# Performance work log

Measured on AMD Instinct MI355X. Metric: run time of the kernel, lower is better.

Reference implementation:

```python
import jax, jax.numpy as jnp
import numpy as np

B, N, D_IN, D_HID, D_OUT = 8, 512, 4608, 4608, 1152
DROP = 0.1
INV_SQRT2 = 0.7071067811865476
INV_SQRT_2PI = 0.3989422804014327


def _clean(s):
    # nan -> 1e-5, inf -> 1.0 (matches torch.where chain)
    return jnp.where(jnp.isnan(s), jnp.asarray(1e-5, s.dtype),
                     jnp.where(jnp.isinf(s), jnp.asarray(1.0, s.dtype), s))


def kl_regularizer(w_mu, w_sigma):
    d = w_mu.shape[0]
    ws = jax.nn.softplus(w_sigma)  # log(1+exp(w_sigma))
    return 0.5 * jnp.mean(d * ws + jnp.sum(w_mu * w_mu, axis=0) - d - d * jnp.log(ws))


def vdp_linear(mu_in, Sigma_in, w_mu, w_sigma):
    mu_out = jnp.matmul(mu_in, w_mu)                                 # [B,N,U]
    kl = kl_regularizer(w_mu, w_sigma)
    W_Sigma = jax.nn.softplus(w_sigma)                               # [U]
    Sigma_1 = jnp.matmul(Sigma_in, w_mu * w_mu)                      # w^T Sigma_in w (diag)
    Sigma_2 = jnp.sum(mu_in * mu_in, axis=-1, keepdims=True) * W_Sigma
    Sigma_3 = jnp.sum(Sigma_in, axis=-1, keepdims=True) * W_Sigma
    return mu_out, _clean(Sigma_1 + Sigma_2 + Sigma_3), kl


def vdp_gelu(mu_in, Sigma_in):
    # exact (erf) gelu and its analytic derivative: Phi(x) + x*phi(x)
    cdf = 0.5 * (1.0 + jax.lax.erf(mu_in * INV_SQRT2))
    pdf = jnp.exp(-0.5 * mu_in * mu_in) * INV_SQRT_2PI
    grad = cdf + mu_in * pdf
    return mu_in * cdf, grad * grad * Sigma_in


def vdp_dropout(mu_in, Sigma_in, mask):
    keep = 1.0 - DROP
    m = mask.astype(mu_in.dtype)
    mu_out = mu_in * m / keep                       # torch F.dropout scaling
    Sigma_out = Sigma_in * m / mu_in.shape[-1]      # kept Sigma values (unscaled), / units
    return mu_out, _clean(Sigma_out)


def setup_inputs() -> dict:
    key = jax.random.key(0)
    k = jax.random.split(key, 8)
    mu_in = jax.random.normal(k[0], (B, N, D_IN), dtype=jnp.float32)
    sigma_in = jax.random.uniform(k[1], (B, N, D_IN), dtype=jnp.float32)
    mask1 = jax.random.bernoulli(k[2], 1.0 - DROP, (B, N, D_HID))
    mask2 = jax.random.bernoulli(k[3], 1.0 - DROP, (B, N, D_OUT))
    w_mu1 = 0.05 * jax.random.normal(k[4], (D_IN, D_HID), dtype=jnp.float32)
    w_sigma1 = jnp.full((D_HID,), -4.6, dtype=jnp.float32)
    w_mu2 = 0.05 * jax.random.normal(k[5], (D_HID, D_OUT), dtype=jnp.float32)
    w_sigma2 = jnp.full((D_OUT,), -4.6, dtype=jnp.float32)
    return {"mu_in": mu_in, "sigma_in": sigma_in, "mask1": mask1, "mask2": mask2,
            "w_mu1": w_mu1, "w_sigma1": w_sigma1, "w_mu2": w_mu2, "w_sigma2": w_sigma2}


def reference(mu_in, sigma_in, mask1, mask2, w_mu1, w_sigma1, w_mu2, w_sigma2):
    mu, sig, kl1 = vdp_linear(mu_in, sigma_in, w_mu1, w_sigma1)
    mu, sig = vdp_gelu(mu, sig)
    mu, sig = vdp_dropout(mu, sig, mask1)
    mu, sig, kl2 = vdp_linear(mu, sig, w_mu2, w_sigma2)
    mu, sig = vdp_dropout(mu, sig, mask2)
    return mu, _clean(sig), kl1 + kl2
```

## Files before the change

kernel.cpp:

```cpp
#include <hip/hip_runtime.h>
#include <cstdint>
#include <cstddef>

static constexpr int Mrows = 4096;
static constexpr int K1 = 4608;
static constexpr int N1 = 4608;
static constexpr int N2 = 1152;
static constexpr int SPLITK = 2;
static constexpr int NPART1 = (K1 / 32) * (N1 / 32);
static constexpr int NPART2 = (K1 / 32) * (N2 / 32);

static constexpr float SC_SIGIN = 256.f;
static constexpr float SC_WSQ   = 4096.f;
static constexpr float SC_SIG3  = 16384.f;
static constexpr float DSC_L1   = 1.f / (SC_SIGIN * SC_WSQ);
static constexpr float DSC_L2   = 1.f / (SC_SIG3 * SC_WSQ);

typedef float  f32x4  __attribute__((ext_vector_type(4)));
typedef __bf16 bf16x8 __attribute__((ext_vector_type(8)));

__device__ __forceinline__ unsigned short f2bf(float f) {
  unsigned int u = __float_as_uint(f);
  u += 0x7fffu + ((u >> 16) & 1u);
  return (unsigned short)(u >> 16);
}
__device__ __forceinline__ float bf2f(unsigned short h) {
  return __uint_as_float(((unsigned int)h) << 16);
}
__device__ __forceinline__ float cleanf(float s) {
  if (__builtin_isnan(s)) return 1e-5f;
  if (__builtin_isinf(s)) return 1.0f;
  return s;
}
__device__ __forceinline__ unsigned int pk_fp8x4(float a, float b, float c, float d) {
  int p = __builtin_amdgcn_cvt_pk_fp8_f32(a, b, 0, false);
  p = __builtin_amdgcn_cvt_pk_fp8_f32(c, d, p, true);
  return (unsigned int)p;
}

__global__ __launch_bounds__(256) void prep_in(
    const float* __restrict__ mu, const float* __restrict__ sg,
    unsigned short* __restrict__ A1, unsigned char* __restrict__ As,
    float* __restrict__ rmu2, float* __restrict__ rsg)
{
  const int row = blockIdx.x;
  const int tid = threadIdx.x;
  const float4* mup = (const float4*)(mu + (size_t)row * K1);
  const float4* sgp = (const float4*)(sg + (size_t)row * K1);
  ushort4* a1p = (ushort4*)(A1 + (size_t)row * K1);
  unsigned int* asp = (unsigned int*)(As + (size_t)row * K1);
  float smu = 0.f, ssg = 0.f;
  for (int j = tid; j < K1 / 4; j += 256) {
    float4 m4 = mup[j];
    float4 s4 = sgp[j];
    smu += m4.x*m4.x + m4.y*m4.y + m4.z*m4.z + m4.w*m4.w;
    ssg += s4.x + s4.y + s4.z + s4.w;
    a1p[j] = make_ushort4(f2bf(m4.x), f2bf(m4.y), f2bf(m4.z), f2bf(m4.w));
    asp[j] = pk_fp8x4(s4.x * SC_SIGIN, s4.y * SC_SIGIN, s4.z * SC_SIGIN, s4.w * SC_SIGIN);
  }
  __shared__ float red[2][4];
  for (int off = 32; off; off >>= 1) {
    smu += __shfl_down(smu, off);
    ssg += __shfl_down(ssg, off);
  }
  const int lane = tid & 63, wv = tid >> 6;
  if (!lane) { red[0][wv] = smu; red[1][wv] = ssg; }
  __syncthreads();
  if (tid == 0) {
    rmu2[row] = red[0][0] + red[0][1] + red[0][2] + red[0][3];
    rsg[row]  = red[1][0] + red[1][1] + red[1][2] + red[1][3];
  }
}

__global__ __launch_bounds__(256) void prep_w(
    const float* __restrict__ w, unsigned short* __restrict__ Bt,
    unsigned char* __restrict__ Bsq, float* __restrict__ partials,
    int K, int N)
{
  __shared__ float t[32][33];
  const int kt = blockIdx.x * 32;
  const int nt = blockIdx.y * 32;
  const int tx = threadIdx.x & 31;
  const int ty = threadIdx.x >> 5;
  float loc = 0.f;
#pragma unroll
  for (int i = 0; i < 32; i += 8) {
    float v = w[(size_t)(kt + ty + i) * N + (nt + tx)];
    t[ty + i][tx] = v;
    loc += v * v;
  }
  __syncthreads();
#pragma unroll
  for (int i = 0; i < 32; i += 8) {
    float v = t[tx][ty + i];
    size_t o = (size_t)(nt + ty + i) * K + (kt + tx);
    Bt[o]  = f2bf(v);
    Bsq[o] = (unsigned char)(__builtin_amdgcn_cvt_pk_fp8_f32(v * v * SC_WSQ, 0.f, 0, false) & 0xff);
  }
  __shared__ float red[4];
  for (int off = 32; off; off >>= 1) loc += __shfl_down(loc, off);
  const int lane = threadIdx.x & 63, wv = threadIdx.x >> 6;
  if (!lane) red[wv] = loc;
  __syncthreads();
  if (threadIdx.x == 0)
    partials[blockIdx.y * gridDim.x + blockIdx.x] = red[0] + red[1] + red[2] + red[3];
}

__global__ __launch_bounds__(256) void kl_prep(
    const float* __restrict__ wsig1, const float* __restrict__ wsig2,
    const float* __restrict__ part1, const float* __restrict__ part2,
    float* __restrict__ ws1, float* __restrict__ ws2, float* __restrict__ outkl)
{
  const int tid = threadIdx.x;
  float s1 = 0.f, l1 = 0.f, s2 = 0.f, l2 = 0.f, q1 = 0.f, q2 = 0.f;
  for (int j = tid; j < N1; j += 256) {
    float x = wsig1[j];
    float sp = (x > 20.f) ? x : log1pf(expf(x));
    ws1[j] = sp; s1 += sp; l1 += logf(sp);
  }
  for (int j = tid; j < N2; j += 256) {
    float x = wsig2[j];
    float sp = (x > 20.f) ? x : log1pf(expf(x));
    ws2[j] = sp; s2 += sp; l2 += logf(sp);
  }
  for (int j = tid; j < NPART1; j += 256) q1 += part1[j];
  for (int j = tid; j < NPART2; j += 256) q2 += part2[j];
  __shared__ float red[6][4];
  for (int off = 32; off; off >>= 1) {
    s1 += __shfl_down(s1, off); l1 += __shfl_down(l1, off);
    s2 += __shfl_down(s2, off); l2 += __shfl_down(l2, off);
    q1 += __shfl_down(q1, off); q2 += __shfl_down(q2, off);
  }
  const int lane = tid & 63, wv = tid >> 6;
  if (!lane) {
    red[0][wv] = s1; red[1][wv] = l1; red[2][wv] = s2;
    red[3][wv] = l2; red[4][wv] = q1; red[5][wv] = q2;
  }
  __syncthreads();
  if (tid == 0) {
    float S1v = red[0][0] + red[0][1] + red[0][2] + red[0][3];
    float L1v = red[1][0] + red[1][1] + red[1][2] + red[1][3];
    float S2v = red[2][0] + red[2][1] + red[2][2] + red[2][3];
    float L2v = red[3][0] + red[3][1] + red[3][2] + red[3][3];
    float Q1v = red[4][0] + red[4][1] + red[4][2] + red[4][3];
    float Q2v = red[5][0] + red[5][1] + red[5][2] + red[5][3];
    const float d = 4608.f;
    float kl1 = 0.5f * (d * (S1v / (float)N1) + Q1v / (float)N1 - d - d * (L1v / (float)N1));
    float kl2 = 0.5f * (d * (S2v / (float)N2) + Q2v / (float)N2 - d - d * (L2v / (float)N2));
    outkl[0] = kl1 + kl2;
  }
}

#define GLD16(gp, lp) __builtin_amdgcn_global_load_lds( \
    (__attribute__((address_space(1))) void*)(unsigned short*)(gp), \
    (__attribute__((address_space(3))) void*)(lp), 16, 0, 0)

__device__ __forceinline__ void storeC(float v, float* p) { *p = v; }
__device__ __forceinline__ void storeC(float v, unsigned short* p) { *p = f2bf(v); }

template <typename CT>
__global__ __launch_bounds__(256) void gemm_bt2(
    const unsigned short* __restrict__ Aa, const unsigned char* __restrict__ As8,
    const unsigned short* __restrict__ Ba, const unsigned char* __restrict__ Bq8,
    CT* __restrict__ Ca, CT* __restrict__ Cs,
    int M, int N, int Kstride, int Klen, float sdescale)
{
  __shared__ __align__(16) char smem[32768];
  const int tid = threadIdx.x;
  const int lane = tid & 63;
  const int wave = tid >> 6;

  const int which = blockIdx.z & 1;
  const int slice = blockIdx.z >> 1;

  const int m0 = blockIdx.y * 128;
  const int n0 = blockIdx.x * 128;
  const int wm = (wave & 1) * 64;
  const int wn = (wave >> 1) * 64;

  const int fm = lane & 15;
  const int kq = lane >> 4;

  f32x4 acc[4][4];
#pragma unroll
  for (int i = 0; i < 4; i++)
#pragma unroll
    for (int j = 0; j < 4; j++) acc[i][j] = (f32x4){0.f, 0.f, 0.f, 0.f};

  if (which == 0) {
    const unsigned short* A  = Aa + (size_t)slice * Klen;
    const unsigned short* Bt = Ba + (size_t)slice * Klen;
    unsigned short* lA = (unsigned short*)smem;
    unsigned short* lB = (unsigned short*)(smem + 16384);

    const int c0 = tid, c1 = tid + 256;
    const int r0s = c0 >> 2, k0s = (c0 & 3) ^ ((r0s >> 1) & 3);
    const int r1s = c1 >> 2, k1s = (c1 & 3) ^ ((r1s >> 1) & 3);
    const unsigned short* gA0 = A + (size_t)(m0 + r0s) * Kstride + k0s * 8;
    const unsigned short* gA1 = A + (size_t)(m0 + r1s) * Kstride + k1s * 8;
    const unsigned short* gB0 = Bt + (size_t)(n0 + r0s) * Kstride + k0s * 8;
    const unsigned short* gB1 = Bt + (size_t)(n0 + r1s) * Kstride + k1s * 8;

    int aoff[4], boff[4];
#pragma unroll
    for (int i = 0; i < 4; i++) {
      int ra = wm + i * 16 + fm;
      aoff[i] = ra * 32 + ((kq ^ ((ra >> 1) & 3)) * 8);
      int rb = wn + i * 16 + fm;
      boff[i] = rb * 32 + ((kq ^ ((rb >> 1) & 3)) * 8);
    }

    GLD16(gA0, &lA[c0 * 8]); GLD16(gA1, &lA[c1 * 8]);
    GLD16(gB0, &lB[c0 * 8]); GLD16(gB1, &lB[c1 * 8]);
    gA0 += 32; gA1 += 32; gB0 += 32; gB1 += 32;

    const int ksteps = Klen >> 5;
    int cur = 0;
    for (int kt = 0; kt < ksteps; kt++) {
      __syncthreads();
      if (kt + 1 < ksteps) {
        const int nb = cur ^ 1;
        GLD16(gA0, &lA[nb * 4096 + c0 * 8]); GLD16(gA1, &lA[nb * 4096 + c1 * 8]);
        GLD16(gB0, &lB[nb * 4096 + c0 * 8]); GLD16(gB1, &lB[nb * 4096 + c1 * 8]);
        gA0 += 32; gA1 += 32; gB0 += 32; gB1 += 32;
      }
      bf16x8 af[4], bfr[4];
#pragma unroll
      for (int i = 0; i < 4; i++) af[i] = *(const bf16x8*)&lA[cur * 4096 + aoff[i]];
#pragma unroll
      for (int i = 0; i < 4; i++) bfr[i] = *(const bf16x8*)&lB[cur * 4096 + boff[i]];
#pragma unroll
      for (int i = 0; i < 4; i++)
#pragma unroll
        for (int j = 0; j < 4; j++)
          acc[i][j] = __builtin_amdgcn_mfma_f32_16x16x32_bf16(af[i], bfr[j], acc[i][j], 0, 0, 0);
      cur ^= 1;
    }

    CT* C = Ca + (size_t)slice * M * N;
    const int rr = (lane >> 4) * 4;
    const int cc = lane & 15;
#pragma unroll
    for (int i = 0; i < 4; i++) {
      const int grow = m0 + wm + i * 16 + rr;
#pragma unroll
      for (int j = 0; j < 4; j++) {
        const int gcol = n0 + wn + j * 16 + cc;
        CT* cp = C + (size_t)grow * N + gcol;
#pragma unroll
        for (int r = 0; r < 4; r++) storeC(acc[i][j][r], cp + (size_t)r * N);
      }
    }
  } else {
    const unsigned char* A  = As8 + (size_t)slice * Klen;
    const unsigned char* Bt = Bq8 + (size_t)slice * Klen;
    char* lA = smem;
    char* lB = smem + 16384;

    const int s1 = tid, s2 = tid + 256;
    const int r1 = s1 & 127, h1 = s1 >> 7;
    const int r2 = s2 & 127, h2 = s2 >> 7;
    const unsigned char* gA0 = A + (size_t)(m0 + r1) * Kstride + h1 * 16;
    const unsigned char* gA1 = A + (size_t)(m0 + r2) * Kstride + h2 * 16;
    const unsigned char* gB0 = Bt + (size_t)(n0 + r1) * Kstride + h1 * 16;
    const unsigned char* gB1 = Bt + (size_t)(n0 + r2) * Kstride + h2 * 16;

    int aoff8[2][4], boff8[2][4];
#pragma unroll
    for (int hh = 0; hh < 2; hh++)
#pragma unroll
      for (int i = 0; i < 4; i++) {
        const int c = hh * 4 + kq;
        aoff8[hh][i] = (c >> 1) * 2048 + (wm + i * 16 + fm) * 16 + (c & 1) * 8;
        boff8[hh][i] = (c >> 1) * 2048 + (wn + i * 16 + fm) * 16 + (c & 1) * 8;
      }

    GLD16(gA0, lA + s1 * 16); GLD16(gA1, lA + s2 * 16);
    GLD16(gB0, lB + s1 * 16); GLD16(gB1, lB + s2 * 16);
    gA0 += 64; gA1 += 64; gB0 += 64; gB1 += 64;

    const int ksteps = Klen >> 6;
    int cur = 0;
    for (int kt = 0; kt < ksteps; kt++) {
      __syncthreads();
      if (kt + 1 < ksteps) {
        const int nb = cur ^ 1;
        GLD16(gA0, lA + nb * 8192 + s1 * 16); GLD16(gA1, lA + nb * 8192 + s2 * 16);
        GLD16(gB0, lB + nb * 8192 + s1 * 16); GLD16(gB1, lB + nb * 8192 + s2 * 16);
        gA0 += 64; gA1 += 64; gB0 += 64; gB1 += 64;
      }
#pragma unroll
      for (int hh = 0; hh < 2; hh++) {
        long av[4], bv[4];
#pragma unroll
        for (int i = 0; i < 4; i++) av[i] = *(const long*)(lA + cur * 8192 + aoff8[hh][i]);
#pragma unroll
        for (int i = 0; i < 4; i++) bv[i] = *(const long*)(lB + cur * 8192 + boff8[hh][i]);
#pragma unroll
        for (int i = 0; i < 4; i++)
#pragma unroll
          for (int j = 0; j < 4; j++)
            acc[i][j] = __builtin_amdgcn_mfma_f32_16x16x32_fp8_fp8(av[i], bv[j], acc[i][j], 0, 0, 0);
      }
      cur ^= 1;
    }

    CT* C = Cs + (size_t)slice * M * N;
    const int rr = (lane >> 4) * 4;
    const int cc = lane & 15;
#pragma unroll
    for (int i = 0; i < 4; i++) {
      const int grow = m0 + wm + i * 16 + rr;
#pragma unroll
      for (int j = 0; j < 4; j++) {
        const int gcol = n0 + wn + j * 16 + cc;
        CT* cp = C + (size_t)grow * N + gcol;
#pragma unroll
        for (int r = 0; r < 4; r++) storeC(acc[i][j][r] * sdescale, cp + (size_t)r * N);
      }
    }
  }
}

__global__ __launch_bounds__(256) void mid_kernel(
    const unsigned short* __restrict__ mu1, const unsigned short* __restrict__ S1,
    const int* __restrict__ mask1, const float* __restrict__ ws1,
    const float* __restrict__ rmu2, const float* __restrict__ rsg,
    unsigned short* __restrict__ A2, unsigned char* __restrict__ As2,
    float* __restrict__ r2mu, float* __restrict__ r2sg)
{
  const int row = blockIdx.x;
  const int tid = threadIdx.x;
  const float rterm = rmu2[row] + rsg[row];
  const ushort4* mup = (const ushort4*)(mu1 + (size_t)row * N1);
  const ushort4* s1p = (const ushort4*)(S1 + (size_t)row * N1);
  const int4* mkp = (const int4*)(mask1 + (size_t)row * N1);
  const float4* wsp = (const float4*)ws1;
  ushort4* a2p = (ushort4*)(A2 + (size_t)row * N1);
  unsigned int* as2p = (unsigned int*)(As2 + (size_t)row * N1);
  float smu = 0.f, ssg = 0.f;
  for (int j = tid; j < N1 / 4; j += 256) {
    ushort4 m4 = mup[j]; ushort4 s4 = s1p[j]; int4 k4 = mkp[j]; float4 w4 = wsp[j];
    float xv[4] = {bf2f(m4.x), bf2f(m4.y), bf2f(m4.z), bf2f(m4.w)};
    float Sv[4] = {bf2f(s4.x), bf2f(s4.y), bf2f(s4.z), bf2f(s4.w)};
    float wv[4] = {w4.x, w4.y, w4.z, w4.w};
    int   kv[4] = {k4.x, k4.y, k4.z, k4.w};
    unsigned short oa[4];
    float os[4];
#pragma unroll
    for (int t = 0; t < 4; t++) {
      float sig1 = cleanf(Sv[t] + rterm * wv[t]);
      float x = xv[t];
      float cdf = 0.5f * (1.f + erff(x * 0.70710678118654752f));
      float pdf = expf(-0.5f * x * x) * 0.3989422804014327f;
      float g = cdf + x * pdf;
      float mu2v = x * cdf;
      float sig2 = g * g * sig1;
      float mm = (float)kv[t];
      float mu3 = mu2v * mm * (1.f / 0.9f);
      float sig3 = cleanf(sig2 * mm * (1.f / 4608.f));
      smu += mu3 * mu3;
      ssg += sig3;
      oa[t] = f2bf(mu3);
      os[t] = sig3 * SC_SIG3;
    }
    a2p[j] = make_ushort4(oa[0], oa[1], oa[2], oa[3]);
    as2p[j] = pk_fp8x4(os[0], os[1], os[2], os[3]);
  }
  __shared__ float red[2][4];
  for (int off = 32; off; off >>= 1) {
    smu += __shfl_down(smu, off);
    ssg += __shfl_down(ssg, off);
  }
  const int lane = tid & 63, wv2 = tid >> 6;
  if (!lane) { red[0][wv2] = smu; red[1][wv2] = ssg; }
  __syncthreads();
  if (tid == 0) {
    r2mu[row] = red[0][0] + red[0][1] + red[0][2] + red[0][3];
    r2sg[row] = red[1][0] + red[1][1] + red[1][2] + red[1][3];
  }
}

__global__ __launch_bounds__(256) void final_kernel(
    const float* __restrict__ pmu, const float* __restrict__ psig,
    const int* __restrict__ mask2, const float* __restrict__ ws2,
    const float* __restrict__ r2mu, const float* __restrict__ r2sg,
    float* __restrict__ out_mu, float* __restrict__ out_sig)
{
  const int row = blockIdx.x;
  const int tid = threadIdx.x;
  const float rterm = r2mu[row] + r2sg[row];
  const size_t sstride = (size_t)Mrows * N2;
  const float4* mup0 = (const float4*)(pmu + (size_t)row * N2);
  const float4* sbp0 = (const float4*)(psig + (size_t)row * N2);
  const int4* mkp = (const int4*)(mask2 + (size_t)row * N2);
  const float4* wsp = (const float4*)ws2;
  float4* omp = (float4*)(out_mu + (size_t)row * N2);
  float4* osp = (float4*)(out_sig + (size_t)row * N2);
  const size_t s4 = sstride / 4;
  for (int j = tid; j < N2 / 4; j += 256) {
    float4 m4 = mup0[j];
    float4 sb = sbp0[j];
#pragma unroll
    for (int s = 1; s < SPLITK; s++) {
      float4 a = mup0[j + s * s4];
      float4 b = sbp0[j + s * s4];
      m4.x += a.x; m4.y += a.y; m4.z += a.z; m4.w += a.w;
      sb.x += b.x; sb.y += b.y; sb.z += b.z; sb.w += b.w;
    }
    int4 k4 = mkp[j]; float4 w4 = wsp[j];
    float mo[4], so[4];
    float mv[4] = {m4.x, m4.y, m4.z, m4.w};
    float sv[4] = {sb.x, sb.y, sb.z, sb.w};
    float wv[4] = {w4.x, w4.y, w4.z, w4.w};
    int   kv[4] = {k4.x, k4.y, k4.z, k4.w};
#pragma unroll
    for (int t = 0; t < 4; t++) {
      float sig4 = cleanf(sv[t] + rterm * wv[t]);
      float mm = (float)kv[t];
      float mu5 = mv[t] * mm * (1.f / 0.9f);
      float sig5 = cleanf(sig4 * mm * (1.f / 1152.f));
      mo[t] = mu5;
      so[t] = cleanf(sig5);
    }
    omp[j] = make_float4(mo[0], mo[1], mo[2], mo[3]);
    osp[j] = make_float4(so[0], so[1], so[2], so[3]);
  }
}

extern "C" void kernel_launch(void* const* d_in, const int* in_sizes, int n_in,
                              void* d_out, int out_size, void* d_ws, size_t ws_size,
                              hipStream_t stream)
{
  const float* mu_in = (const float*)d_in[0];
  const float* sg_in = (const float*)d_in[1];
  const int* mask1 = (const int*)d_in[2];
  const int* mask2 = (const int*)d_in[3];
  const float* w_mu1 = (const float*)d_in[4];
  const float* wsig1 = (const float*)d_in[5];
  const float* w_mu2 = (const float*)d_in[6];
  const float* wsig2 = (const float*)d_in[7];
  float* out = (float*)d_out;

  char* ws = (char*)d_ws;
  const size_t oA1  = 0;
  const size_t oAs  = oA1  + (size_t)37748736;
  const size_t oB1t = oAs  + (size_t)37748736;
  const size_t oB1q = oB1t + (size_t)42467328;
  const size_t oB2t = oB1q + (size_t)42467328;
  const size_t oB2q = oB2t + (size_t)10616832;
  const size_t oMu1 = oB2q + (size_t)10616832;
  const size_t oS1  = oMu1 + (size_t)37748736;
  const size_t oVec = oS1  + (size_t)37748736;

  unsigned short* A1    = (unsigned short*)(ws + oA1);
  unsigned char*  As8   = (unsigned char*)(ws + oAs);
  unsigned short* B1t   = (unsigned short*)(ws + oB1t);
  unsigned char*  B1q8  = (unsigned char*)(ws + oB1q);
  unsigned short* B2t   = (unsigned short*)(ws + oB2t);
  unsigned char*  B2q8  = (unsigned char*)(ws + oB2q);
  unsigned short* mu1b  = (unsigned short*)(ws + oMu1);
  unsigned short* S1b16 = (unsigned short*)(ws + oS1);
  float* pmu  = (float*)(ws + oB1t);
  float* psig = (float*)(ws + oMu1);

  float* rmu2 = (float*)(ws + oVec);
  float* rsg  = rmu2 + Mrows;
  float* r2mu = rsg + Mrows;
  float* r2sg = r2mu + Mrows;
  float* ws1v = r2sg + Mrows;
  float* ws2v = ws1v + N1;
  float* part1 = ws2v + N2;
  float* part2 = part1 + NPART1;

  prep_in<<<Mrows, 256, 0, stream>>>(mu_in, sg_in, A1, As8, rmu2, rsg);
  prep_w<<<dim3(K1 / 32, N1 / 32), 256, 0, stream>>>(w_mu1, B1t, B1q8, part1, K1, N1);
  prep_w<<<dim3(K1 / 32, N2 / 32), 256, 0, stream>>>(w_mu2, B2t, B2q8, part2, K1, N2);
  kl_prep<<<1, 256, 0, stream>>>(wsig1, wsig2, part1, part2, ws1v, ws2v,
                                 out + (size_t)2 * Mrows * N2);

  gemm_bt2<unsigned short><<<dim3(N1 / 128, Mrows / 128, 2), 256, 0, stream>>>(
      A1, As8, B1t, B1q8, mu1b, S1b16, Mrows, N1, K1, K1, DSC_L1);

  mid_kernel<<<Mrows, 256, 0, stream>>>(mu1b, S1b16, mask1, ws1v, rmu2, rsg,
                                        A1, As8, r2mu, r2sg);

  gemm_bt2<float><<<dim3(N2 / 128, Mrows / 128, 2 * SPLITK), 256, 0, stream>>>(
      A1, As8, B2t, B2q8, pmu, psig, Mrows, N2, K1, K1 / SPLITK, DSC_L2);

  final_kernel<<<Mrows, 256, 0, stream>>>(pmu, psig, mask2, ws2v, r2mu, r2sg,
                                          out, out + (size_t)Mrows * N2);
  (void)in_sizes; (void)n_in; (void)out_size; (void)ws_size;
}
```

Baseline: 969.8 us.

## Replace first-layer GEMM with 256x256-tile bf16 kernel for both mu and sigma

The first layer's mean and variance GEMMs now run through a new 512-thread kernel with 256x256 output tiles, 128 KB of double-buffered LDS, swizzled direct-to-LDS loads and interleaved bf16 MFMA phases. The sigma path changes from fp8 to bf16 operands, so prep_in and prep_w now write bf16 sigma_in and bf16 squared weights. The larger tiles raise data reuse per block and use one MFMA type for both products. In exchange, sigma operand traffic doubles, and the bigger tile yields fewer blocks, which may leave compute units underused.

Result: faster. 913.8 us (-5.8%).

```diff
diff --git a/kernel.cpp b/kernel.cpp
--- a/kernel.cpp
+++ b/kernel.cpp
@@ -10,10 +10,8 @@
 static constexpr int NPART1 = (K1 / 32) * (N1 / 32);
 static constexpr int NPART2 = (K1 / 32) * (N2 / 32);
 
-static constexpr float SC_SIGIN = 256.f;
 static constexpr float SC_WSQ   = 4096.f;
 static constexpr float SC_SIG3  = 16384.f;
-static constexpr float DSC_L1   = 1.f / (SC_SIGIN * SC_WSQ);
 static constexpr float DSC_L2   = 1.f / (SC_SIG3 * SC_WSQ);
 
 typedef float  f32x4  __attribute__((ext_vector_type(4)));
@@ -40,7 +38,7 @@
 
 __global__ __launch_bounds__(256) void prep_in(
     const float* __restrict__ mu, const float* __restrict__ sg,
-    unsigned short* __restrict__ A1, unsigned char* __restrict__ As,
+    unsigned short* __restrict__ A1, unsigned short* __restrict__ As16,
     float* __restrict__ rmu2, float* __restrict__ rsg)
 {
   const int row = blockIdx.x;
@@ -48,7 +46,7 @@
   const float4* mup = (const float4*)(mu + (size_t)row * K1);
   const float4* sgp = (const float4*)(sg + (size_t)row * K1);
   ushort4* a1p = (ushort4*)(A1 + (size_t)row * K1);
-  unsigned int* asp = (unsigned int*)(As + (size_t)row * K1);
+  ushort4* asp = (ushort4*)(As16 + (size_t)row * K1);
   float smu = 0.f, ssg = 0.f;
   for (int j = tid; j < K1 / 4; j += 256) {
     float4 m4 = mup[j];
@@ -56,7 +54,7 @@
     smu += m4.x*m4.x + m4.y*m4.y + m4.z*m4.z + m4.w*m4.w;
     ssg += s4.x + s4.y + s4.z + s4.w;
     a1p[j] = make_ushort4(f2bf(m4.x), f2bf(m4.y), f2bf(m4.z), f2bf(m4.w));
-    asp[j] = pk_fp8x4(s4.x * SC_SIGIN, s4.y * SC_SIGIN, s4.z * SC_SIGIN, s4.w * SC_SIGIN);
+    asp[j] = make_ushort4(f2bf(s4.x), f2bf(s4.y), f2bf(s4.z), f2bf(s4.w));
   }
   __shared__ float red[2][4];
   for (int off = 32; off; off >>= 1) {
@@ -74,8 +72,8 @@
 
 __global__ __launch_bounds__(256) void prep_w(
     const float* __restrict__ w, unsigned short* __restrict__ Bt,
-    unsigned char* __restrict__ Bsq, float* __restrict__ partials,
-    int K, int N)
+    void* __restrict__ Bsq, float* __restrict__ partials,
+    int K, int N, int sq16)
 {
   __shared__ float t[32][33];
   const int kt = blockIdx.x * 32;
@@ -94,8 +92,12 @@
   for (int i = 0; i < 32; i += 8) {
     float v = t[tx][ty + i];
     size_t o = (size_t)(nt + ty + i) * K + (kt + tx);
-    Bt[o]  = f2bf(v);
-    Bsq[o] = (unsigned char)(__builtin_amdgcn_cvt_pk_fp8_f32(v * v * SC_WSQ, 0.f, 0, false) & 0xff);
+    Bt[o] = f2bf(v);
+    if (sq16)
+      ((unsigned short*)Bsq)[o] = f2bf(v * v);
+    else
+      ((unsigned char*)Bsq)[o] =
+          (unsigned char)(__builtin_amdgcn_cvt_pk_fp8_f32(v * v * SC_WSQ, 0.f, 0, false) & 0xff);
   }
   __shared__ float red[4];
   for (int off = 32; off; off >>= 1) loc += __shfl_down(loc, off);
@@ -154,6 +156,127 @@
 #define GLD16(gp, lp) __builtin_amdgcn_global_load_lds( \
     (__attribute__((address_space(1))) void*)(unsigned short*)(gp), \
     (__attribute__((address_space(3))) void*)(lp), 16, 0, 0)
+
+#define G256_PHASE(I0, STAGE_STMT, TAIL_STMT)                                   \
+  {                                                                             \
+    bf16x8 Af[2][2];                                                            \
+    _Pragma("unroll")                                                           \
+    for (int ii = 0; ii < 2; ++ii) {                                            \
+      Af[ii][0] = *(const bf16x8*)(cA + (I0 + ii) * 2048 + x0);                 \
+      Af[ii][1] = *(const bf16x8*)(cA + (I0 + ii) * 2048 + x1);                 \
+    }                                                                           \
+    STAGE_STMT;                                                                 \
+    __builtin_amdgcn_s_barrier();                                               \
+    asm volatile("s_waitcnt lgkmcnt(0)" ::: "memory");                          \
+    __builtin_amdgcn_s_setprio(1);                                              \
+    _Pragma("unroll")                                                           \
+    for (int ii = 0; ii < 2; ++ii)                                              \
+      _Pragma("unroll")                                                         \
+      for (int j = 0; j < 4; ++j) {                                             \
+        acc[I0 + ii][j] = __builtin_amdgcn_mfma_f32_16x16x32_bf16(              \
+            Af[ii][0], Bf[j][0], acc[I0 + ii][j], 0, 0, 0);                     \
+        acc[I0 + ii][j] = __builtin_amdgcn_mfma_f32_16x16x32_bf16(              \
+            Af[ii][1], Bf[j][1], acc[I0 + ii][j], 0, 0, 0);                     \
+      }                                                                         \
+    __builtin_amdgcn_s_setprio(0);                                              \
+    TAIL_STMT;                                                                  \
+    __builtin_amdgcn_s_barrier();                                               \
+  }
+
+__global__ __launch_bounds__(512, 2) void gemm256(
+    const unsigned short* __restrict__ Amu, const unsigned short* __restrict__ Asg,
+    const unsigned short* __restrict__ Bmu, const unsigned short* __restrict__ Bsq,
+    unsigned short* __restrict__ Cmu, unsigned short* __restrict__ Csg)
+{
+  __shared__ __align__(16) char smem[131072];
+  char* lA = smem;
+  char* lB = smem + 65536;
+
+  const int tid  = threadIdx.x;
+  const int lane = tid & 63;
+  const int wave = tid >> 6;
+  const int which = blockIdx.z;
+  const unsigned short* Ag = which ? Asg : Amu;
+  const unsigned short* Bg = which ? Bsq : Bmu;
+  unsigned short* Cg = which ? Csg : Cmu;
+
+  const int m0 = blockIdx.y * 256;
+  const int n0 = blockIdx.x * 256;
+  const int wm = (wave >> 2) * 128;
+  const int wn = (wave & 3) * 64;
+  const int fm = lane & 15;
+  const int kq = lane >> 4;
+
+  const int rbase = tid >> 3;
+  const int gg = (tid & 7) ^ (rbase & 7);
+  const unsigned short* gA0 = Ag + (size_t)(m0 + rbase) * K1 + gg * 8;
+  const unsigned short* gB0 = Bg + (size_t)(n0 + rbase) * K1 + gg * 8;
+
+  auto stA = [&](int buf, int h, int kt2) {
+    const unsigned short* g = gA0 + (size_t)h * 128 * K1 + kt2 * 64;
+    char* l = lA + buf * 32768 + h * 16384 + tid * 16;
+    GLD16(g, l);
+    GLD16(g + (size_t)64 * K1, l + 8192);
+  };
+  auto stB = [&](int buf, int h, int kt2) {
+    const unsigned short* g = gB0 + (size_t)h * 128 * K1 + kt2 * 64;
+    char* l = lB + buf * 32768 + h * 16384 + tid * 16;
+    GLD16(g, l);
+    GLD16(g + (size_t)64 * K1, l + 8192);
+  };
+
+  const int ab = (wave >> 2) * 16384 + fm * 128;
+  const int bb = ((wave >> 1) & 1) * 16384 + (wave & 1) * 8192 + fm * 128;
+  const int x0 = ((0 * 4 + kq) ^ (fm & 7)) * 16;
+  const int x1 = ((1 * 4 + kq) ^ (fm & 7)) * 16;
+
+  f32x4 acc[8][4];
+#pragma unroll
+  for (int i = 0; i < 8; ++i)
+#pragma unroll
+    for (int j = 0; j < 4; ++j) acc[i][j] = (f32x4){0.f, 0.f, 0.f, 0.f};
+
+  stB(0, 0, 0); stB(0, 1, 0);
+  stA(0, 0, 0); stA(0, 1, 0);
+  stB(1, 0, 1); stB(1, 1, 1);
+  asm volatile("s_waitcnt vmcnt(4)" ::: "memory");
+  __builtin_amdgcn_s_barrier();
+
+  const int ksteps = K1 / 64;
+  for (int kt = 0; kt < ksteps; ++kt) {
+    const int cur = kt & 1;
+    const char* cA = lA + cur * 32768 + ab;
+    const char* cB = lB + cur * 32768 + bb;
+
+    bf16x8 Bf[4][2];
+#pragma unroll
+    for (int j = 0; j < 4; ++j) {
+      Bf[j][0] = *(const bf16x8*)(cB + j * 2048 + x0);
+      Bf[j][1] = *(const bf16x8*)(cB + j * 2048 + x1);
+    }
+
+    G256_PHASE(0, if (kt + 1 < ksteps) stA(cur ^ 1, 0, kt + 1), )
+    G256_PHASE(2, if (kt + 1 < ksteps) stA(cur ^ 1, 1, kt + 1), )
+    G256_PHASE(4, if (kt + 2 < ksteps) stB(cur, 0, kt + 2), )
+    G256_PHASE(6, if (kt + 2 < ksteps) stB(cur, 1, kt + 2),
+               if (kt < ksteps - 2) asm volatile("s_waitcnt vmcnt(4)" ::: "memory");
+               else                 asm volatile("s_waitcnt vmcnt(0)" ::: "memory"))
+  }
+
+  const int rr = (lane >> 4) * 4;
+  const int cc = lane & 15;
+#pragma unroll
+  for (int i = 0; i < 8; ++i) {
+    const int grow = m0 + wm + i * 16 + rr;
+#pragma unroll
+    for (int j = 0; j < 4; ++j) {
+      const int gcol = n0 + wn + j * 16 + cc;
+      unsigned short* cp = Cg + (size_t)grow * N1 + gcol;
+#pragma unroll
+      for (int r = 0; r < 4; ++r) cp[(size_t)r * N1] = f2bf(acc[i][j][r]);
+    }
+  }
+}
 
 __device__ __forceinline__ void storeC(float v, float* p) { *p = v; }
 __device__ __forceinline__ void storeC(float v, unsigned short* p) { *p = f2bf(v); }
@@ -453,14 +576,15 @@
   const size_t oS1  = oMu1 + (size_t)37748736;
   const size_t oVec = oS1  + (size_t)37748736;
 
-  unsigned short* A1    = (unsigned short*)(ws + oA1);
-  unsigned char*  As8   = (unsigned char*)(ws + oAs);
-  unsigned short* B1t   = (unsigned short*)(ws + oB1t);
-  unsigned char*  B1q8  = (unsigned char*)(ws + oB1q);
-  unsigned short* B2t   = (unsigned short*)(ws + oB2t);
-  unsigned char*  B2q8  = (unsigned char*)(ws + oB2q);
-  unsigned short* mu1b  = (unsigned short*)(ws + oMu1);
-  unsigned short* S1b16 = (unsigned short*)(ws + oS1);
+  unsigned short* A1     = (unsigned short*)(ws + oA1);
+  unsigned short* As16   = (unsigned short*)(ws + oAs);
+  unsigned char*  As8    = (unsigned char*)(ws + oAs);
+  unsigned short* B1t    = (unsigned short*)(ws + oB1t);
+  unsigned short* B1sq16 = (unsigned short*)(ws + oB1q);
+  unsigned short* B2t    = (unsigned short*)(ws + oB2t);
+  unsigned char*  B2q8   = (unsigned char*)(ws + oB2q);
+  unsigned short* mu1b   = (unsigned short*)(ws + oMu1);
+  unsigned short* S1b16  = (unsigned short*)(ws + oS1);
   float* pmu  = (float*)(ws + oB1t);
   float* psig = (float*)(ws + oMu1);
 
@@ -473,14 +597,14 @@
   float* part1 = ws2v + N2;
   float* part2 = part1 + NPART1;
 
-  prep_in<<<Mrows, 256, 0, stream>>>(mu_in, sg_in, A1, As8, rmu2, rsg);
-  prep_w<<<dim3(K1 / 32, N1 / 32), 256, 0, stream>>>(w_mu1, B1t, B1q8, part1, K1, N1);
-  prep_w<<<dim3(K1 / 32, N2 / 32), 256, 0, stream>>>(w_mu2, B2t, B2q8, part2, K1, N2);
+  prep_in<<<Mrows, 256, 0, stream>>>(mu_in, sg_in, A1, As16, rmu2, rsg);
+  prep_w<<<dim3(K1 / 32, N1 / 32), 256, 0, stream>>>(w_mu1, B1t, (void*)B1sq16, part1, K1, N1, 1);
+  prep_w<<<dim3(K1 / 32, N2 / 32), 256, 0, stream>>>(w_mu2, B2t, (void*)B2q8, part2, K1, N2, 0);
   kl_prep<<<1, 256, 0, stream>>>(wsig1, wsig2, part1, part2, ws1v, ws2v,
                                  out + (size_t)2 * Mrows * N2);
 
-  gemm_bt2<unsigned short><<<dim3(N1 / 128, Mrows / 128, 2), 256, 0, stream>>>(
-      A1, As8, B1t, B1q8, mu1b, S1b16, Mrows, N1, K1, K1, DSC_L1);
+  gemm256<<<dim3(N1 / 256, Mrows / 256, 2), 512, 0, stream>>>(
+      A1, As16, B1t, B1sq16, mu1b, S1b16);
 
   mid_kernel<<<Mrows, 256, 0, stream>>>(mu1b, S1b16, mask1, ws1v, rmu2, rsg,
                                         A1, As8, r2mu, r2sg);
```
